# Performance work log

Hardware: AMD Instinct MI355X
Metric: run time of the kernel (lower is better)

The kernel has to match this reference:

```python
import jax, jax.numpy as jnp
import numpy as np
from functools import partial

ITERS = 100
EPSILON = 0.8
TAU = 1.02
FEATURE_DIM = 256
MATCHED_THRESHOLD = 0.2
B, D, N0, N1 = 1, 256, 2048, 2048


def log_optimal_transport_extended(scores, alpha, iters, epsilon, tau):
    b, m, n = scores.shape
    dt = scores.dtype
    ms = jnp.asarray(m, dt)
    ns = jnp.asarray(n, dt)
    bins0 = jnp.broadcast_to(alpha, (b, m, 1)).astype(dt)
    bins1 = jnp.broadcast_to(alpha, (b, 1, n)).astype(dt)
    corner = jnp.broadcast_to(alpha, (b, 1, 1)).astype(dt)
    # couplings: [b, m+1, n+1] score matrix augmented with dustbin row/col
    couplings = jnp.concatenate([
        jnp.concatenate([scores, bins0], axis=-1),
        jnp.concatenate([bins1, corner], axis=-1)], axis=1)
    norm = -jnp.log(ms + ns)
    log_mu = jnp.concatenate([jnp.full((m,), norm, dt), (jnp.log(ns) + norm)[None]])
    log_nu = jnp.concatenate([jnp.full((n,), norm, dt), (jnp.log(ms) + norm)[None]])
    log_mu = jnp.broadcast_to(log_mu[None], (b, m + 1))
    log_nu = jnp.broadcast_to(log_nu[None], (b, n + 1))

    def step(carry, _):
        u, v = carry
        u_new = (log_mu - jax.scipy.special.logsumexp(couplings + v[:, None, :], axis=2)) / tau
        u = u + epsilon * (u_new - u)
        v_new = (log_nu - jax.scipy.special.logsumexp(couplings + u[:, :, None], axis=1)) / tau
        v = v + epsilon * (v_new - v)
        return (u, v), None

    u0 = jnp.zeros_like(log_mu)
    v0 = jnp.zeros_like(log_nu)
    (u, v), _ = jax.lax.scan(jax.checkpoint(step), (u0, v0), None, length=iters)
    Z = couplings + u[:, :, None] + v[:, None, :]
    return Z - norm


def reference(mdesc0, mdesc1, bin_score):
    # mdesc0: [b, d, n], mdesc1: [b, d, m]
    sim = jnp.einsum('bdn,bdm->bnm', mdesc0, mdesc1)
    scores = sim / np.float32(np.sqrt(FEATURE_DIM))
    Z = log_optimal_transport_extended(scores, bin_score, ITERS, EPSILON, TAU)
    inner = Z[:, :-1, :-1]                       # [b, m, n]
    m, n = inner.shape[1], inner.shape[2]
    max0_vals = inner.max(axis=2)
    indices0 = inner.argmax(axis=2)              # [b, m] int
    indices1 = inner.argmax(axis=1)              # [b, n] int
    mutual0 = jnp.arange(m)[None, :] == jnp.take_along_axis(indices1, indices0, axis=1)
    mutual1 = jnp.arange(n)[None, :] == jnp.take_along_axis(indices0, indices1, axis=1)
    zero = jnp.zeros((), inner.dtype)
    mscores0 = jnp.where(mutual0, jnp.exp(max0_vals), zero)
    mscores1 = jnp.where(mutual1, jnp.take_along_axis(mscores0, indices1, axis=1), zero)
    valid0 = mutual0 & (mscores0 > MATCHED_THRESHOLD)
    valid1 = mutual1 & jnp.take_along_axis(valid0, indices1, axis=1)
    i0 = jnp.where(valid0, indices0, -1)
    i1 = jnp.where(valid1, indices1, -1)
    return (jnp.exp(Z[0]), i0[0], i1[0], mscores0[0], mscores1[0])


def setup_inputs() -> dict:
    key = jax.random.key(0)
    k0, k1 = jax.random.split(key)
    mdesc0 = jax.random.normal(k0, (B, D, N0), dtype=jnp.float32)
    mdesc1 = jax.random.normal(k1, (B, D, N1), dtype=jnp.float32)
    bin_score = jnp.ones((), dtype=jnp.float32)  # learned dustbin score, init 1.0
    return {"mdesc0": mdesc0, "mdesc1": mdesc1, "bin_score": bin_score}
```

## Files before the change

kernel.cpp:

```cpp
#include <hip/hip_runtime.h>
#include <hip/hip_bf16.h>
#include <math.h>

#define D        256
#define NINNER   2048
#define NROW     2049
#define SP       2064
#define ITERS_N  100
#define EPS_F    0.8f
#define TAU_F    1.02f
#define NB       256
#define NT       256

typedef unsigned long long u64;

#define PSTRIDE  2112u

#define SZ_MAT   (2049u * 2064u)
#define OFF_E    0u
#define OFF_F    SZ_MAT
#define OFF_WUP  (2u * SZ_MAT)
#define OFF_WVP  (OFF_WUP + 4u * PSTRIDE)
#define OFF_MAX0 (OFF_WVP + 4u * PSTRIDE)
#define OFF_IDX0 (OFF_MAX0 + 2048u)
#define OFF_IDX1 (OFF_IDX0 + 2048u)
#define OFF_MS0  (OFF_IDX1 + 2048u)
#define OFF_VLD0 (OFF_MS0 + 2048u)

#define OOFF_Z   0u
#define OOFF_I0  (2049u * 2049u)
#define OOFF_I1  (OOFF_I0 + 2048u)
#define OOFF_S0  (OOFF_I1 + 2048u)
#define OOFF_S1  (OOFF_S0 + 2048u)

__device__ __forceinline__ float    pair_val(u64 x) { return __uint_as_float((unsigned)x); }
__device__ __forceinline__ unsigned pair_tag(u64 x) { return (unsigned)(x >> 32); }
__device__ __forceinline__ u64 make_pair(float v, unsigned t) {
    return ((u64)t << 32) | (u64)__float_as_uint(v);
}

__global__ __launch_bounds__(256) void k_gemm(const float* __restrict__ A,
                                              const float* __restrict__ Bm,
                                              float* __restrict__ E) {
    __shared__ float As[8][64];
    __shared__ float Bs[8][64];
    const int tid = threadIdx.x;
    const int tx = tid & 15, ty = tid >> 4;
    const int row0 = blockIdx.y * 64, col0 = blockIdx.x * 64;
    float acc[4][4] = {};
    const int lr = tid >> 6, lc = tid & 63;
    for (int k0 = 0; k0 < D; k0 += 8) {
        As[lr][lc]     = A[(k0 + lr) * NINNER + row0 + lc];
        As[lr + 4][lc] = A[(k0 + lr + 4) * NINNER + row0 + lc];
        Bs[lr][lc]     = Bm[(k0 + lr) * NINNER + col0 + lc];
        Bs[lr + 4][lc] = Bm[(k0 + lr + 4) * NINNER + col0 + lc];
        __syncthreads();
#pragma unroll
        for (int kk = 0; kk < 8; ++kk) {
            const float4 av = *(const float4*)&As[kk][ty * 4];
            const float4 bv = *(const float4*)&Bs[kk][tx * 4];
            const float a_[4] = {av.x, av.y, av.z, av.w};
            const float b_[4] = {bv.x, bv.y, bv.z, bv.w};
#pragma unroll
            for (int r = 0; r < 4; ++r)
#pragma unroll
                for (int c = 0; c < 4; ++c)
                    acc[r][c] = fmaf(a_[r], b_[c], acc[r][c]);
        }
        __syncthreads();
    }
    const int row = row0 + ty * 4, col = col0 + tx * 4;
#pragma unroll
    for (int r = 0; r < 4; ++r) {
        float4 o;
        o.x = expf(acc[r][0] * 0.0625f);
        o.y = expf(acc[r][1] * 0.0625f);
        o.z = expf(acc[r][2] * 0.0625f);
        o.w = expf(acc[r][3] * 0.0625f);
        *(float4*)(E + (size_t)(row + r) * SP + col) = o;
    }
}

__global__ __launch_bounds__(256) void k_init(float* __restrict__ E,
                                              u64* __restrict__ wvb0,
                                              const float* __restrict__ alpha) {
    const int t = blockIdx.x * 256 + threadIdx.x;
    const float ea = expf(alpha[0]);
    if (t < NINNER) E[(size_t)t * SP + NINNER] = ea;
    if (t <= NINNER) E[(size_t)NINNER * SP + t] = ea;
    if (t <= NINNER) wvb0[t] = make_pair(1.0f, 0u);
}

__global__ __launch_bounds__(256) void k_transpose(const float* __restrict__ E,
                                                   float* __restrict__ F) {
    __shared__ float tle[32][33];
    const int tx = threadIdx.x & 31;
    const int ty4 = (threadIdx.x >> 5) * 4;
    const int bx = blockIdx.x * 32, by = blockIdx.y * 32;
#pragma unroll
    for (int k = 0; k < 4; ++k) {
        const int i = by + ty4 + k, j = bx + tx;
        if (i < NROW && j < NROW) tle[ty4 + k][tx] = E[(size_t)i * SP + j];
    }
    __syncthreads();
#pragma unroll
    for (int k = 0; k < 4; ++k) {
        const int j = bx + ty4 + k, i = by + tx;
        if (i < NROW && j < NROW) F[(size_t)j * SP + i] = tle[tx][ty4 + k];
    }
}

__device__ __forceinline__ void poll8(u64* buf, int tid, unsigned want, float* w) {
    for (;;) {
        u64 a0 = __hip_atomic_load(buf + 0 * 256 + tid, __ATOMIC_RELAXED, __HIP_MEMORY_SCOPE_AGENT);
        u64 a1 = __hip_atomic_load(buf + 1 * 256 + tid, __ATOMIC_RELAXED, __HIP_MEMORY_SCOPE_AGENT);
        u64 a2 = __hip_atomic_load(buf + 2 * 256 + tid, __ATOMIC_RELAXED, __HIP_MEMORY_SCOPE_AGENT);
        u64 a3 = __hip_atomic_load(buf + 3 * 256 + tid, __ATOMIC_RELAXED, __HIP_MEMORY_SCOPE_AGENT);
        u64 a4 = __hip_atomic_load(buf + 4 * 256 + tid, __ATOMIC_RELAXED, __HIP_MEMORY_SCOPE_AGENT);
        u64 a5 = __hip_atomic_load(buf + 5 * 256 + tid, __ATOMIC_RELAXED, __HIP_MEMORY_SCOPE_AGENT);
        u64 a6 = __hip_atomic_load(buf + 6 * 256 + tid, __ATOMIC_RELAXED, __HIP_MEMORY_SCOPE_AGENT);
        u64 a7 = __hip_atomic_load(buf + 7 * 256 + tid, __ATOMIC_RELAXED, __HIP_MEMORY_SCOPE_AGENT);
        const bool ok = (pair_tag(a0) == want) & (pair_tag(a1) == want)
                      & (pair_tag(a2) == want) & (pair_tag(a3) == want)
                      & (pair_tag(a4) == want) & (pair_tag(a5) == want)
                      & (pair_tag(a6) == want) & (pair_tag(a7) == want);
        if (ok) {
            w[0] = pair_val(a0); w[1] = pair_val(a1); w[2] = pair_val(a2); w[3] = pair_val(a3);
            w[4] = pair_val(a4); w[5] = pair_val(a5); w[6] = pair_val(a6); w[7] = pair_val(a7);
            return;
        }
        __builtin_amdgcn_s_sleep(1);
    }
}

__device__ __forceinline__ float poll_bin(u64* buf, unsigned want) {
    for (;;) {
        u64 d = __hip_atomic_load(buf + NINNER, __ATOMIC_RELAXED, __HIP_MEMORY_SCOPE_AGENT);
        if (pair_tag(d) == want) return pair_val(d);
        __builtin_amdgcn_s_sleep(1);
    }
}

__global__ __launch_bounds__(256, 1) void k_sinkhorn(const float* __restrict__ E,
                                                     const float* __restrict__ F,
                                                     u64* wub, u64* wvb,
                                                     const float* __restrict__ alpha) {
    const int b = blockIdx.x, tid = threadIdx.x;
    const int lane = tid & 63, wid = tid >> 6;
    const int base = b * 8;
    const bool lastb = (b == NB - 1);
    __shared__ float red[2][4][9];

    const float norm = -8.317766166719343f;
    const float logbin = 7.624618986159398f + norm;
    const float ea = expf(alpha[0]);

    float eR[8][8], fR[8][8];
#pragma unroll
    for (int r = 0; r < 8; ++r) {
        const float* rowE = E + (size_t)(base + r) * SP;
        const float* rowF = F + (size_t)(base + r) * SP;
#pragma unroll
        for (int q = 0; q < 8; ++q) {
            eR[r][q] = rowE[q * 256 + tid];
            fR[r][q] = rowF[q * 256 + tid];
        }
    }

    float u = 0.0f, v = 0.0f;
    float ub = 0.0f, vb = 0.0f;

    for (int it = 0; it < ITERS_N; ++it) {
        {
            u64* src = wvb + (size_t)(it & 1) * PSTRIDE;
            u64* dst = wub + (size_t)((it + 1) & 1) * PSTRIDE;
            const unsigned want = (unsigned)it, prod = (unsigned)(it + 1);
            float w[8];
            poll8(src, tid, want, w);
            const float wd = (tid == 0) ? poll_bin(src, want) : 0.0f;
            float p[8];
#pragma unroll
            for (int r = 0; r < 8; ++r) {
                float s = ea * wd;
#pragma unroll
                for (int q = 0; q < 8; ++q) s = fmaf(eR[r][q], w[q], s);
                p[r] = s;
            }
            float t = w[0] + w[1] + w[2] + w[3] + w[4] + w[5] + w[6] + w[7] + wd;
#pragma unroll
            for (int r = 0; r < 8; ++r) {
                float s = p[r];
#pragma unroll
                for (int m = 1; m < 64; m <<= 1) s += __shfl_xor(s, m, 64);
                if (lane == 0) red[0][wid][r] = s;
            }
#pragma unroll
            for (int m = 1; m < 64; m <<= 1) t += __shfl_xor(t, m, 64);
            if (lane == 0) red[0][wid][8] = t;
            __syncthreads();
            if (tid < 8) {
                const float S = red[0][0][tid] + red[0][1][tid] + red[0][2][tid] + red[0][3][tid];
                const float unew = (norm - logf(S)) / TAU_F;
                u = u + EPS_F * (unew - u);
                __hip_atomic_store(dst + base + tid, make_pair(expf(u), prod),
                                   __ATOMIC_RELAXED, __HIP_MEMORY_SCOPE_AGENT);
            }
            if (lastb && tid == 8) {
                const float S = ea * (red[0][0][8] + red[0][1][8] + red[0][2][8] + red[0][3][8]);
                const float unew = (logbin - logf(S)) / TAU_F;
                ub = ub + EPS_F * (unew - ub);
                __hip_atomic_store(dst + NINNER, make_pair(expf(ub), prod),
                                   __ATOMIC_RELAXED, __HIP_MEMORY_SCOPE_AGENT);
            }
        }
        {
            u64* src = wub + (size_t)((it + 1) & 1) * PSTRIDE;
            u64* dst = wvb + (size_t)((it + 1) & 1) * PSTRIDE;
            const unsigned want = (unsigned)(it + 1), prod = (unsigned)(it + 1);
            float w[8];
            poll8(src, tid, want, w);
            const float wd = (tid == 0) ? poll_bin(src, want) : 0.0f;
            float p[8];
#pragma unroll
            for (int r = 0; r < 8; ++r) {
                float s = ea * wd;
#pragma unroll
                for (int q = 0; q < 8; ++q) s = fmaf(fR[r][q], w[q], s);
                p[r] = s;
            }
            float t = w[0] + w[1] + w[2] + w[3] + w[4] + w[5] + w[6] + w[7] + wd;
#pragma unroll
            for (int r = 0; r < 8; ++r) {
                float s = p[r];
#pragma unroll
                for (int m = 1; m < 64; m <<= 1) s += __shfl_xor(s, m, 64);
                if (lane == 0) red[1][wid][r] = s;
            }
#pragma unroll
            for (int m = 1; m < 64; m <<= 1) t += __shfl_xor(t, m, 64);
            if (lane == 0) red[1][wid][8] = t;
            __syncthreads();
            if (tid < 8) {
                const float T = red[1][0][tid] + red[1][1][tid] + red[1][2][tid] + red[1][3][tid];
                const float vnew = (norm - logf(T)) / TAU_F;
                v = v + EPS_F * (vnew - v);
                __hip_atomic_store(dst + base + tid, make_pair(expf(v), prod),
                                   __ATOMIC_RELAXED, __HIP_MEMORY_SCOPE_AGENT);
            }
            if (lastb && tid == 8) {
                const float T = ea * (red[1][0][8] + red[1][1][8] + red[1][2][8] + red[1][3][8]);
                const float vnew = (logbin - logf(T)) / TAU_F;
                vb = vb + EPS_F * (vnew - vb);
                __hip_atomic_store(dst + NINNER, make_pair(expf(vb), prod),
                                   __ATOMIC_RELAXED, __HIP_MEMORY_SCOPE_AGENT);
            }
        }
    }
}

__global__ __launch_bounds__(256) void k_rowpass(const float* __restrict__ E,
                                                 const float2* __restrict__ wup,
                                                 const float2* __restrict__ wvp,
                                                 float* __restrict__ out,
                                                 float* __restrict__ max0,
                                                 int* __restrict__ idx0) {
    const int i = blockIdx.x;
    const int tid = threadIdx.x;
    const int lane = tid & 63, wid = tid >> 6;
    const float wui = wup[i].x * 4096.0f;
    const float* row = E + (size_t)i * SP;
    float best = -1.0f; int bidx = 0;
    for (int j = tid; j < NROW; j += 256) {
        const float val = row[j] * wvp[j].x * wui;
        out[(size_t)i * NROW + j] = val;
        if (j < NINNER && val > best) { best = val; bidx = j; }
    }
    if (i < NINNER) {
        __shared__ float sb[4]; __shared__ int si[4];
#pragma unroll
        for (int m = 1; m < 64; m <<= 1) {
            const float ob = __shfl_xor(best, m, 64);
            const int   oi = __shfl_xor(bidx, m, 64);
            if (ob > best || (ob == best && oi < bidx)) { best = ob; bidx = oi; }
        }
        if (lane == 0) { sb[wid] = best; si[wid] = bidx; }
        __syncthreads();
        if (tid == 0) {
            for (int k = 1; k < 4; ++k)
                if (sb[k] > best || (sb[k] == best && si[k] < bidx)) { best = sb[k]; bidx = si[k]; }
            max0[i] = best; idx0[i] = bidx;
        }
    }
}

__global__ __launch_bounds__(256) void k_colpass(const float* __restrict__ F,
                                                 const float2* __restrict__ wup,
                                                 int* __restrict__ idx1) {
    const int j = blockIdx.x;
    const int tid = threadIdx.x;
    const int lane = tid & 63, wid = tid >> 6;
    const float* row = F + (size_t)j * SP;
    float best = -1.0f; int bidx = 0;
    for (int i = tid; i < NINNER; i += 256) {
        const float q = row[i] * wup[i].x;
        if (q > best) { best = q; bidx = i; }
    }
    __shared__ float sb[4]; __shared__ int si[4];
#pragma unroll
    for (int m = 1; m < 64; m <<= 1) {
        const float ob = __shfl_xor(best, m, 64);
        const int   oi = __shfl_xor(bidx, m, 64);
        if (ob > best || (ob == best && oi < bidx)) { best = ob; bidx = oi; }
    }
    if (lane == 0) { sb[wid] = best; si[wid] = bidx; }
    __syncthreads();
    if (tid == 0) {
        for (int k = 1; k < 4; ++k)
            if (sb[k] > best || (sb[k] == best && si[k] < bidx)) { best = sb[k]; bidx = si[k]; }
        idx1[j] = bidx;
    }
}

__global__ __launch_bounds__(256) void k_match0(const float* __restrict__ max0,
                                                const int* __restrict__ idx0,
                                                const int* __restrict__ idx1,
                                                float* __restrict__ ms0,
                                                int* __restrict__ vld0,
                                                float* __restrict__ out) {
    const int i = blockIdx.x * 256 + threadIdx.x;
    if (i >= NINNER) return;
    const int j = idx0[i];
    const bool mut = (idx1[j] == i);
    const float ms = mut ? max0[i] : 0.0f;
    const bool val = mut && (ms > 0.2f);
    ms0[i] = ms; vld0[i] = val ? 1 : 0;
    out[OOFF_I0 + i] = val ? (float)j : -1.0f;
    out[OOFF_S0 + i] = ms;
}
__global__ __launch_bounds__(256) void k_match1(const int* __restrict__ idx0,
                                                const int* __restrict__ idx1,
                                                const float* __restrict__ ms0,
                                                const int* __restrict__ vld0,
                                                float* __restrict__ out) {
    const int j = blockIdx.x * 256 + threadIdx.x;
    if (j >= NINNER) return;
    const int i = idx1[j];
    const bool mut = (idx0[i] == j);
    const float ms = mut ? ms0[i] : 0.0f;
    const bool val = mut && (vld0[i] != 0);
    out[OOFF_I1 + j] = val ? (float)i : -1.0f;
    out[OOFF_S1 + j] = ms;
}

extern "C" void kernel_launch(void* const* d_in, const int* in_sizes, int n_in,
                              void* d_out, int out_size, void* d_ws, size_t ws_size,
                              hipStream_t stream) {
    const float* A     = (const float*)d_in[0];
    const float* Bm    = (const float*)d_in[1];
    const float* alpha = (const float*)d_in[2];

    float* ws = (float*)d_ws;
    float* E    = ws + OFF_E;
    float* F    = ws + OFF_F;
    u64*   wub  = (u64*)(ws + OFF_WUP);
    u64*   wvb  = (u64*)(ws + OFF_WVP);
    float* max0 = ws + OFF_MAX0;
    int*   idx0 = (int*)(ws + OFF_IDX0);
    int*   idx1 = (int*)(ws + OFF_IDX1);
    float* ms0  = ws + OFF_MS0;
    int*   vld0 = (int*)(ws + OFF_VLD0);
    float* out  = (float*)d_out;

    k_gemm<<<dim3(32, 32), 256, 0, stream>>>(A, Bm, E);
    k_init<<<dim3(16), 256, 0, stream>>>(E, wvb, alpha);
    k_transpose<<<dim3(65, 65), 256, 0, stream>>>(E, F);
    k_sinkhorn<<<dim3(NB), NT, 0, stream>>>(E, F, wub, wvb, alpha);
    k_rowpass<<<dim3(NROW), 256, 0, stream>>>(E, (const float2*)wub, (const float2*)wvb,
                                              out, max0, idx0);
    k_colpass<<<dim3(NINNER), 256, 0, stream>>>(F, (const float2*)wub, idx1);
    k_match0<<<dim3(8), 256, 0, stream>>>(max0, idx0, idx1, ms0, vld0, out);
    k_match1<<<dim3(8), 256, 0, stream>>>(idx0, idx1, ms0, vld0, out);
}
```

Baseline: 952.9 us.

## Fuse transpose into GEMM epilogue, merge row/col passes, tighten polling

The GEMM epilogue now writes both E and its transpose F directly, so the separate transpose kernel is gone and k_init fills F's dustbin entries too. The row-pass and column-pass kernels are merged into one k_finish launch. The Sinkhorn polling loops drop s_sleep and only reload slots that are not ready yet, aiming to cut inter-block sync latency. The transposed F stores are strided float4 writes, which coalesce poorly, and busy polling without sleep adds memory traffic.

```diff
diff --git a/kernel.cpp b/kernel.cpp
--- a/kernel.cpp
+++ b/kernel.cpp
@@ -41,7 +41,8 @@
 
 __global__ __launch_bounds__(256) void k_gemm(const float* __restrict__ A,
                                               const float* __restrict__ Bm,
-                                              float* __restrict__ E) {
+                                              float* __restrict__ E,
+                                              float* __restrict__ F) {
     __shared__ float As[8][64];
     __shared__ float Bs[8][64];
     const int tid = threadIdx.x;
@@ -69,75 +70,64 @@
         }
         __syncthreads();
     }
+    float o[4][4];
+#pragma unroll
+    for (int r = 0; r < 4; ++r)
+#pragma unroll
+        for (int c = 0; c < 4; ++c)
+            o[r][c] = expf(acc[r][c] * 0.0625f);
     const int row = row0 + ty * 4, col = col0 + tx * 4;
 #pragma unroll
-    for (int r = 0; r < 4; ++r) {
-        float4 o;
-        o.x = expf(acc[r][0] * 0.0625f);
-        o.y = expf(acc[r][1] * 0.0625f);
-        o.z = expf(acc[r][2] * 0.0625f);
-        o.w = expf(acc[r][3] * 0.0625f);
-        *(float4*)(E + (size_t)(row + r) * SP + col) = o;
-    }
+    for (int r = 0; r < 4; ++r)
+        *(float4*)(E + (size_t)(row + r) * SP + col)
+            = make_float4(o[r][0], o[r][1], o[r][2], o[r][3]);
+#pragma unroll
+    for (int c = 0; c < 4; ++c)
+        *(float4*)(F + (size_t)(col + c) * SP + row)
+            = make_float4(o[0][c], o[1][c], o[2][c], o[3][c]);
 }
 
 __global__ __launch_bounds__(256) void k_init(float* __restrict__ E,
+                                              float* __restrict__ F,
                                               u64* __restrict__ wvb0,
                                               const float* __restrict__ alpha) {
     const int t = blockIdx.x * 256 + threadIdx.x;
     const float ea = expf(alpha[0]);
-    if (t < NINNER) E[(size_t)t * SP + NINNER] = ea;
-    if (t <= NINNER) E[(size_t)NINNER * SP + t] = ea;
-    if (t <= NINNER) wvb0[t] = make_pair(1.0f, 0u);
-}
-
-__global__ __launch_bounds__(256) void k_transpose(const float* __restrict__ E,
-                                                   float* __restrict__ F) {
-    __shared__ float tle[32][33];
-    const int tx = threadIdx.x & 31;
-    const int ty4 = (threadIdx.x >> 5) * 4;
-    const int bx = blockIdx.x * 32, by = blockIdx.y * 32;
-#pragma unroll
-    for (int k = 0; k < 4; ++k) {
-        const int i = by + ty4 + k, j = bx + tx;
-        if (i < NROW && j < NROW) tle[ty4 + k][tx] = E[(size_t)i * SP + j];
-    }
-    __syncthreads();
-#pragma unroll
-    for (int k = 0; k < 4; ++k) {
-        const int j = bx + ty4 + k, i = by + tx;
-        if (i < NROW && j < NROW) F[(size_t)j * SP + i] = tle[tx][ty4 + k];
-    }
-}
-
-__device__ __forceinline__ void poll8(u64* buf, int tid, unsigned want, float* w) {
+    if (t < NINNER) {
+        E[(size_t)t * SP + NINNER] = ea;
+        F[(size_t)t * SP + NINNER] = ea;
+    }
+    if (t <= NINNER) {
+        E[(size_t)NINNER * SP + t] = ea;
+        F[(size_t)NINNER * SP + t] = ea;
+        wvb0[t] = make_pair(1.0f, 0u);
+    }
+}
+
+__device__ __forceinline__ void poll8(const u64* buf, int tid, unsigned want, float* w) {
+    u64 a[8];
+#pragma unroll
+    for (int q = 0; q < 8; ++q)
+        a[q] = __hip_atomic_load(buf + q * 256 + tid, __ATOMIC_RELAXED, __HIP_MEMORY_SCOPE_AGENT);
     for (;;) {
-        u64 a0 = __hip_atomic_load(buf + 0 * 256 + tid, __ATOMIC_RELAXED, __HIP_MEMORY_SCOPE_AGENT);
-        u64 a1 = __hip_atomic_load(buf + 1 * 256 + tid, __ATOMIC_RELAXED, __HIP_MEMORY_SCOPE_AGENT);
-        u64 a2 = __hip_atomic_load(buf + 2 * 256 + tid, __ATOMIC_RELAXED, __HIP_MEMORY_SCOPE_AGENT);
-        u64 a3 = __hip_atomic_load(buf + 3 * 256 + tid, __ATOMIC_RELAXED, __HIP_MEMORY_SCOPE_AGENT);
-        u64 a4 = __hip_atomic_load(buf + 4 * 256 + tid, __ATOMIC_RELAXED, __HIP_MEMORY_SCOPE_AGENT);
-        u64 a5 = __hip_atomic_load(buf + 5 * 256 + tid, __ATOMIC_RELAXED, __HIP_MEMORY_SCOPE_AGENT);
-        u64 a6 = __hip_atomic_load(buf + 6 * 256 + tid, __ATOMIC_RELAXED, __HIP_MEMORY_SCOPE_AGENT);
-        u64 a7 = __hip_atomic_load(buf + 7 * 256 + tid, __ATOMIC_RELAXED, __HIP_MEMORY_SCOPE_AGENT);
-        const bool ok = (pair_tag(a0) == want) & (pair_tag(a1) == want)
-                      & (pair_tag(a2) == want) & (pair_tag(a3) == want)
-                      & (pair_tag(a4) == want) & (pair_tag(a5) == want)
-                      & (pair_tag(a6) == want) & (pair_tag(a7) == want);
-        if (ok) {
-            w[0] = pair_val(a0); w[1] = pair_val(a1); w[2] = pair_val(a2); w[3] = pair_val(a3);
-            w[4] = pair_val(a4); w[5] = pair_val(a5); w[6] = pair_val(a6); w[7] = pair_val(a7);
-            return;
-        }
-        __builtin_amdgcn_s_sleep(1);
-    }
-}
-
-__device__ __forceinline__ float poll_bin(u64* buf, unsigned want) {
+        unsigned miss = 0u;
+#pragma unroll
+        for (int q = 0; q < 8; ++q)
+            miss |= (pair_tag(a[q]) != want) ? (1u << q) : 0u;
+        if (!miss) break;
+#pragma unroll
+        for (int q = 0; q < 8; ++q)
+            if (miss & (1u << q))
+                a[q] = __hip_atomic_load(buf + q * 256 + tid, __ATOMIC_RELAXED, __HIP_MEMORY_SCOPE_AGENT);
+    }
+#pragma unroll
+    for (int q = 0; q < 8; ++q) w[q] = pair_val(a[q]);
+}
+
+__device__ __forceinline__ float poll_bin(const u64* buf, unsigned want) {
     for (;;) {
         u64 d = __hip_atomic_load(buf + NINNER, __ATOMIC_RELAXED, __HIP_MEMORY_SCOPE_AGENT);
         if (pair_tag(d) == want) return pair_val(d);
-        __builtin_amdgcn_s_sleep(1);
     }
 }
 
@@ -258,25 +248,53 @@
     }
 }
 
-__global__ __launch_bounds__(256) void k_rowpass(const float* __restrict__ E,
-                                                 const float2* __restrict__ wup,
-                                                 const float2* __restrict__ wvp,
-                                                 float* __restrict__ out,
-                                                 float* __restrict__ max0,
-                                                 int* __restrict__ idx0) {
+__global__ __launch_bounds__(256) void k_finish(const float* __restrict__ E,
+                                                const float* __restrict__ F,
+                                                const float2* __restrict__ wup,
+                                                const float2* __restrict__ wvp,
+                                                float* __restrict__ out,
+                                                float* __restrict__ max0,
+                                                int* __restrict__ idx0,
+                                                int* __restrict__ idx1) {
     const int i = blockIdx.x;
     const int tid = threadIdx.x;
     const int lane = tid & 63, wid = tid >> 6;
-    const float wui = wup[i].x * 4096.0f;
-    const float* row = E + (size_t)i * SP;
-    float best = -1.0f; int bidx = 0;
-    for (int j = tid; j < NROW; j += 256) {
-        const float val = row[j] * wvp[j].x * wui;
-        out[(size_t)i * NROW + j] = val;
-        if (j < NINNER && val > best) { best = val; bidx = j; }
-    }
+    __shared__ float sb[4]; __shared__ int si[4];
+
+    {
+        const float wui = wup[i].x * 4096.0f;
+        const float* row = E + (size_t)i * SP;
+        float best = -1.0f; int bidx = 0;
+        for (int j = tid; j < NROW; j += 256) {
+            const float val = row[j] * wvp[j].x * wui;
+            out[(size_t)i * NROW + j] = val;
+            if (j < NINNER && val > best) { best = val; bidx = j; }
+        }
+        if (i < NINNER) {
+#pragma unroll
+            for (int m = 1; m < 64; m <<= 1) {
+                const float ob = __shfl_xor(best, m, 64);
+                const int   oi = __shfl_xor(bidx, m, 64);
+                if (ob > best || (ob == best && oi < bidx)) { best = ob; bidx = oi; }
+            }
+            if (lane == 0) { sb[wid] = best; si[wid] = bidx; }
+            __syncthreads();
+            if (tid == 0) {
+                for (int k = 1; k < 4; ++k)
+                    if (sb[k] > best || (sb[k] == best && si[k] < bidx)) { best = sb[k]; bidx = si[k]; }
+                max0[i] = best; idx0[i] = bidx;
+            }
+        }
+    }
+
     if (i < NINNER) {
-        __shared__ float sb[4]; __shared__ int si[4];
+        __syncthreads();
+        const float* row = F + (size_t)i * SP;
+        float best = -1.0f; int bidx = 0;
+        for (int r = tid; r < NINNER; r += 256) {
+            const float q = row[r] * wup[r].x;
+            if (q > best) { best = q; bidx = r; }
+        }
 #pragma unroll
         for (int m = 1; m < 64; m <<= 1) {
             const float ob = __shfl_xor(best, m, 64);
@@ -288,36 +306,8 @@
         if (tid == 0) {
             for (int k = 1; k < 4; ++k)
                 if (sb[k] > best || (sb[k] == best && si[k] < bidx)) { best = sb[k]; bidx = si[k]; }
-            max0[i] = best; idx0[i] = bidx;
-        }
-    }
-}
-
-__global__ __launch_bounds__(256) void k_colpass(const float* __restrict__ F,
-                                                 const float2* __restrict__ wup,
-                                                 int* __restrict__ idx1) {
-    const int j = blockIdx.x;
-    const int tid = threadIdx.x;
-    const int lane = tid & 63, wid = tid >> 6;
-    const float* row = F + (size_t)j * SP;
-    float best = -1.0f; int bidx = 0;
-    for (int i = tid; i < NINNER; i += 256) {
-        const float q = row[i] * wup[i].x;
-        if (q > best) { best = q; bidx = i; }
-    }
-    __shared__ float sb[4]; __shared__ int si[4];
-#pragma unroll
-    for (int m = 1; m < 64; m <<= 1) {
-        const float ob = __shfl_xor(best, m, 64);
-        const int   oi = __shfl_xor(bidx, m, 64);
-        if (ob > best || (ob == best && oi < bidx)) { best = ob; bidx = oi; }
-    }
-    if (lane == 0) { sb[wid] = best; si[wid] = bidx; }
-    __syncthreads();
-    if (tid == 0) {
-        for (int k = 1; k < 4; ++k)
-            if (sb[k] > best || (sb[k] == best && si[k] < bidx)) { best = sb[k]; bidx = si[k]; }
-        idx1[j] = bidx;
+            idx1[i] = bidx;
+        }
     }
 }
 
@@ -371,13 +361,11 @@
     int*   vld0 = (int*)(ws + OFF_VLD0);
     float* out  = (float*)d_out;
 
-    k_gemm<<<dim3(32, 32), 256, 0, stream>>>(A, Bm, E);
-    k_init<<<dim3(16), 256, 0, stream>>>(E, wvb, alpha);
-    k_transpose<<<dim3(65, 65), 256, 0, stream>>>(E, F);
+    k_gemm<<<dim3(32, 32), 256, 0, stream>>>(A, Bm, E, F);
+    k_init<<<dim3(16), 256, 0, stream>>>(E, F, wvb, alpha);
     k_sinkhorn<<<dim3(NB), NT, 0, stream>>>(E, F, wub, wvb, alpha);
-    k_rowpass<<<dim3(NROW), 256, 0, stream>>>(E, (const float2*)wub, (const float2*)wvb,
-                                              out, max0, idx0);
-    k_colpass<<<dim3(NINNER), 256, 0, stream>>>(F, (const float2*)wub, idx1);
+    k_finish<<<dim3(NROW), 256, 0, stream>>>(E, F, (const float2*)wub, (const float2*)wvb,
+                                             out, max0, idx0, idx1);
     k_match0<<<dim3(8), 256, 0, stream>>>(max0, idx0, idx1, ms0, vld0, out);
     k_match1<<<dim3(8), 256, 0, stream>>>(idx0, idx1, ms0, vld0, out);
 }
```

Result: faster. 918.7 us (-3.6%).
